# Optimization experiments

Measured on AMD Instinct MI355X. Metric: run time of the kernel, lower is better.

The kernel has to match this reference:

```python
import jax, jax.numpy as jnp
import numpy as np

TEMPERATURE = 0.1
EPS = 1e-8
NEG_INF = -9e15  # matches torch masked_fill value before temperature scaling


def setup_inputs() -> dict:
    key = jax.random.key(0)
    k1, k2 = jax.random.split(key)
    z1 = jax.random.normal(k1, (4096, 512), dtype=jnp.float32)
    z2 = jax.random.normal(k2, (4096, 512), dtype=jnp.float32)
    return {"z1": z1, "z2": z2}


def reference(z1, z2):
    feats = jnp.concatenate([z1, z2], axis=0)          # [2N, D]
    n2 = feats.shape[0]
    norms = jnp.linalg.norm(feats, axis=-1, keepdims=True)
    unit = feats / jnp.maximum(norms, EPS)             # cosine-normalized
    cos_sim = unit @ unit.T                            # [2N, 2N]
    idx = jnp.arange(n2)
    # mask self-similarity on the diagonal
    cos_sim = jnp.where(idx[:, None] == idx[None, :], NEG_INF, cos_sim)
    cos_sim = cos_sim / TEMPERATURE
    # positive for row i sits at column (i + N) mod 2N
    pos = cos_sim[idx, (idx + n2 // 2) % n2]           # [2N]
    nll = -pos + jax.scipy.special.logsumexp(cos_sim, axis=-1)
    return jnp.mean(nll)
```

## Files before the change

kernel.cpp:

```cpp
#include <hip/hip_runtime.h>
#include <hip/hip_bf16.h>
#include <math.h>

#define N2     8192
#define HALF_N 4096
#define DD     512
#define BM     128
#define BN     128
#define BKB    128
#define NKT    (DD / BKB)
#define NB     (N2 / BM)
#define NTRI   (NB * (NB + 1) / 2)

#define U_BYTES    ((size_t)N2 * DD)
#define PART_BYTES ((size_t)NB * N2 * 4)
#define PD_BYTES   ((size_t)HALF_N * 4)

typedef __attribute__((ext_vector_type(4))) float f32x4;
typedef __attribute__((ext_vector_type(4))) int   i32x4;
typedef __attribute__((ext_vector_type(8))) int   i32x8;

#define SCALE1 0x7F7F7F7F

__device__ __forceinline__ void load16_lds(const void* g, void* l) {
    __builtin_amdgcn_global_load_lds(
        (const __attribute__((address_space(1))) void*)g,
        (__attribute__((address_space(3))) void*)l, 16, 0, 0);
}

__global__ __launch_bounds__(256) void prep_kernel(
    const float* __restrict__ z1, const float* __restrict__ z2,
    unsigned char* __restrict__ U, float* __restrict__ out)
{
    const int tid = threadIdx.x;
    if (blockIdx.x == 0 && tid == 0) out[0] = 0.0f;

    const int wave = tid >> 6;
    const int lane = tid & 63;
    const int row  = blockIdx.x * 4 + wave;

    const float* src = (row < HALF_N) ? (z1 + (size_t)row * DD)
                                      : (z2 + (size_t)(row - HALF_N) * DD);
    float4 a = ((const float4*)src)[lane * 2 + 0];
    float4 b = ((const float4*)src)[lane * 2 + 1];
    float ss = a.x*a.x + a.y*a.y + a.z*a.z + a.w*a.w
             + b.x*b.x + b.y*b.y + b.z*b.z + b.w*b.w;
#pragma unroll
    for (int off = 32; off > 0; off >>= 1) ss += __shfl_xor(ss, off);
    const float inv = 1.0f / fmaxf(sqrtf(ss), 1e-8f);

    int lo = __builtin_amdgcn_cvt_pk_fp8_f32(a.x * inv, a.y * inv, 0,  0);
    lo     = __builtin_amdgcn_cvt_pk_fp8_f32(a.z * inv, a.w * inv, lo, 1);
    int hi = __builtin_amdgcn_cvt_pk_fp8_f32(b.x * inv, b.y * inv, 0,  0);
    hi     = __builtin_amdgcn_cvt_pk_fp8_f32(b.z * inv, b.w * inv, hi, 1);

    *(int2*)(U + (size_t)row * DD + lane * 8) = make_int2(lo, hi);
}

__global__ __launch_bounds__(256, 2) void gram_kernel(
    const unsigned char* __restrict__ U, float* __restrict__ partials,
    float* __restrict__ posdot)
{
    __shared__ unsigned char Ash[2][BM][BKB];
    __shared__ unsigned char Bsh[2][BN][BKB];
    __shared__ float racc[2][BM];
    __shared__ float cacc[2][BN];

    const int tid  = threadIdx.x;
    const int wave = tid >> 6;
    const int lane = tid & 63;

    const int t = blockIdx.x;
    int by = (int)((129.0 - sqrt(16641.0 - 8.0 * (double)t)) * 0.5);
    by = min(max(by, 0), NB - 1);
    while (by > 0       && t <  (by * (129 - by)) / 2) --by;
    while (by < NB - 1  && t >= ((by + 1) * (128 - by)) / 2) ++by;
    const int bx = by + (t - (by * (129 - by)) / 2);

    const int wr = wave >> 1;
    const int wc = wave & 1;
    const size_t arow0 = (size_t)by * BM;
    const size_t brow0 = (size_t)bx * BN;

    auto stage = [&](int kt, int buf) {
        const int k0 = kt * BKB;
        const int lr = lane >> 3;
        const int s  = (lane & 7) ^ (lr & 7);
#pragma unroll
        for (int hh = 0; hh < 4; ++hh) {
            const int c = wave * 4 + hh;
            const int r = c * 8 + lr;
            load16_lds(U + (arow0 + r) * DD + k0 + s * 16, &Ash[buf][c * 8][0]);
            load16_lds(U + (brow0 + r) * DD + k0 + s * 16, &Bsh[buf][c * 8][0]);
        }
    };

    f32x4 acc[4][4];
#pragma unroll
    for (int i = 0; i < 4; ++i)
#pragma unroll
        for (int j = 0; j < 4; ++j) acc[i][j] = (f32x4){0.f, 0.f, 0.f, 0.f};

    const int fr   = lane & 15;
    const int quad = lane >> 4;
    const int fr7  = fr & 7;
    const int t0   = (2 * quad) ^ fr7;
    const int t1   = t0 ^ 1;

    stage(0, 0);
    __syncthreads();

    for (int kt = 0; kt < NKT; ++kt) {
        const int buf = kt & 1;
        if (kt + 1 < NKT) stage(kt + 1, buf ^ 1);

        i32x8 af[4], bfr[4];
#pragma unroll
        for (int tt = 0; tt < 4; ++tt) {
            const int ar = wr * 64 + tt * 16 + fr;
            const int br = wc * 64 + tt * 16 + fr;
            i32x4 alo = *(const i32x4*)&Ash[buf][ar][t0 * 16];
            i32x4 ahi = *(const i32x4*)&Ash[buf][ar][t1 * 16];
            i32x4 blo = *(const i32x4*)&Bsh[buf][br][t0 * 16];
            i32x4 bhi = *(const i32x4*)&Bsh[buf][br][t1 * 16];
            af[tt]  = __builtin_shufflevector(alo, ahi, 0, 1, 2, 3, 4, 5, 6, 7);
            bfr[tt] = __builtin_shufflevector(blo, bhi, 0, 1, 2, 3, 4, 5, 6, 7);
        }
#pragma unroll
        for (int ct = 0; ct < 4; ++ct)
#pragma unroll
            for (int rt = 0; rt < 4; ++rt)
                acc[rt][ct] = __builtin_amdgcn_mfma_scale_f32_16x16x128_f8f6f4(
                                  af[rt], bfr[ct], acc[rt][ct],
                                  0, 0,
                                  0, SCALE1,
                                  0, SCALE1);
        __syncthreads();
    }

    const float SC = 14.42695040888963f;
    if (by == bx) {
#pragma unroll
        for (int rt = 0; rt < 4; ++rt) {
            const int lrow = wr * 64 + rt * 16 + quad * 4;
#pragma unroll
            for (int reg = 0; reg < 4; ++reg) {
                const int lr = lrow + reg;
                float s = 0.f;
#pragma unroll
                for (int ct = 0; ct < 4; ++ct) {
                    const int lc = wc * 64 + ct * 16 + fr;
                    const float e = exp2f(acc[rt][ct][reg] * SC);
                    s += (lc == lr) ? 0.f : e;
                }
                s += __shfl_xor(s, 1);
                s += __shfl_xor(s, 2);
                s += __shfl_xor(s, 4);
                s += __shfl_xor(s, 8);
                if (fr == 0) racc[wc][lr] = s;
            }
        }
    } else {
        float csum[4] = {0.f, 0.f, 0.f, 0.f};
#pragma unroll
        for (int rt = 0; rt < 4; ++rt) {
            const int lrow = wr * 64 + rt * 16 + quad * 4;
#pragma unroll
            for (int reg = 0; reg < 4; ++reg) {
                float s = 0.f;
#pragma unroll
                for (int ct = 0; ct < 4; ++ct) {
                    const float e = exp2f(acc[rt][ct][reg] * SC);
                    s += e;
                    csum[ct] += e;
                }
                s += __shfl_xor(s, 1);
                s += __shfl_xor(s, 2);
                s += __shfl_xor(s, 4);
                s += __shfl_xor(s, 8);
                if (fr == 0) racc[wc][lrow + reg] = s;
            }
        }
#pragma unroll
        for (int ct = 0; ct < 4; ++ct) {
            float c = csum[ct];
            c += __shfl_xor(c, 16);
            c += __shfl_xor(c, 32);
            if (quad == 0) cacc[wr][wc * 64 + ct * 16 + fr] = c;
        }
        if (posdot != nullptr && bx == by + 32 && wr == wc) {
#pragma unroll
            for (int rt = 0; rt < 4; ++rt) {
                const int lrow = rt * 16 + quad * 4;
#pragma unroll
                for (int reg = 0; reg < 4; ++reg)
                    if (fr == quad * 4 + reg)
                        posdot[arow0 + wr * 64 + lrow + reg] = acc[rt][rt][reg];
            }
        }
    }
    __syncthreads();

    if (tid < BM) {
        partials[(size_t)bx * N2 + arow0 + tid] = racc[0][tid] + racc[1][tid];
        if (by != bx)
            partials[(size_t)by * N2 + brow0 + tid] = cacc[0][tid] + cacc[1][tid];
    }
}

__global__ __launch_bounds__(256) void finalize_fast(
    const float* __restrict__ partials, const float* __restrict__ posdot,
    float* __restrict__ out)
{
    const int tid = threadIdx.x;
    const int row = blockIdx.x * 256 + tid;
    float s = 0.f;
#pragma unroll 8
    for (int j = 0; j < NB; ++j) s += partials[(size_t)j * N2 + row];
    float nll = -10.0f * posdot[row & (HALF_N - 1)] + logf(s);
#pragma unroll
    for (int off = 32; off > 0; off >>= 1) nll += __shfl_xor(nll, off);
    __shared__ float red[4];
    if ((tid & 63) == 0) red[tid >> 6] = nll;
    __syncthreads();
    if (tid == 0)
        atomicAdd(out, (red[0] + red[1] + red[2] + red[3]) * (1.0f / N2));
}

__device__ __forceinline__ float dec_e4m3(unsigned int b) {
    const int e = (b >> 3) & 15, m = b & 7;
    float v = e ? ldexpf((float)(8 + m), e - 10) : ldexpf((float)m, -9);
    return (b & 0x80u) ? -v : v;
}

__global__ __launch_bounds__(256) void finalize_slow(
    const unsigned char* __restrict__ U, const float* __restrict__ partials,
    float* __restrict__ out)
{
    const int tid  = threadIdx.x;
    const int wave = tid >> 6;
    const int lane = tid & 63;
    const int row  = blockIdx.x * 4 + wave;
    const int prow = (row + HALF_N) & (N2 - 1);

    uint2 xa = *(const uint2*)(U + (size_t)row  * DD + lane * 8);
    uint2 ya = *(const uint2*)(U + (size_t)prow * DD + lane * 8);
    float dot = 0.f;
#pragma unroll
    for (int j = 0; j < 4; ++j)
        dot += dec_e4m3(xa.x >> (8 * j)) * dec_e4m3(ya.x >> (8 * j));
#pragma unroll
    for (int j = 0; j < 4; ++j)
        dot += dec_e4m3(xa.y >> (8 * j)) * dec_e4m3(ya.y >> (8 * j));

    float ps = partials[(size_t)lane * N2 + row];
#pragma unroll
    for (int off = 32; off > 0; off >>= 1) {
        dot += __shfl_xor(dot, off);
        ps  += __shfl_xor(ps,  off);
    }
    __shared__ float part[4];
    if (lane == 0) part[wave] = -10.0f * dot + logf(ps);
    __syncthreads();
    if (tid == 0)
        atomicAdd(out, (part[0] + part[1] + part[2] + part[3]) * (1.0f / N2));
}

extern "C" void kernel_launch(void* const* d_in, const int* in_sizes, int n_in,
                              void* d_out, int out_size, void* d_ws, size_t ws_size,
                              hipStream_t stream)
{
    const float* z1 = (const float*)d_in[0];
    const float* z2 = (const float*)d_in[1];
    float* out      = (float*)d_out;
    unsigned char* U = (unsigned char*)d_ws;
    float* partials  = (float*)((char*)d_ws + U_BYTES);
    float* posdot    = (float*)((char*)d_ws + U_BYTES + PART_BYTES);
    const bool has_pd = ws_size >= U_BYTES + PART_BYTES + PD_BYTES;

    prep_kernel<<<N2 / 4, 256, 0, stream>>>(z1, z2, U, out);
    gram_kernel<<<NTRI, 256, 0, stream>>>(U, partials, has_pd ? posdot : nullptr);
    if (has_pd)
        finalize_fast<<<N2 / 256, 256, 0, stream>>>(partials, posdot, out);
    else
        finalize_slow<<<N2 / 4, 256, 0, stream>>>(U, partials, out);
}
```

Measured before the change: 114.2 us.

## Enlarge Gram tiles to 256x256 with 512-thread blocks and 64x128 wave tiles

Doubles the Gram-matrix block tile from 128x128 to 256x256 and launches 8 waves per block, each computing a 64x128 sub-tile that reuses its A fragments across 8 column tiles. The aim is to cut global-to-LDS and LDS-to-register traffic per MFMA and to shrink the number of triangular tile blocks and partial-sum rows. The triangular index math, diagonal masking, positive-pair extraction and column reductions are adapted to the new geometry. In exchange, LDS use rises to about 128KB per block, so likely only one block fits per CU. The 528 blocks also divide poorly across CUs, which may leave a load-imbalanced tail.

Measured after the change: 220.8 us. 93.3% more time.

```diff
diff --git a/kernel.cpp b/kernel.cpp
--- a/kernel.cpp
+++ b/kernel.cpp
@@ -5,8 +5,7 @@
 #define N2     8192
 #define HALF_N 4096
 #define DD     512
-#define BM     128
-#define BN     128
+#define BM     256
 #define BKB    128
 #define NKT    (DD / BKB)
 #define NB     (N2 / BM)
@@ -57,30 +56,30 @@
     *(int2*)(U + (size_t)row * DD + lane * 8) = make_int2(lo, hi);
 }
 
-__global__ __launch_bounds__(256, 2) void gram_kernel(
+__global__ __launch_bounds__(512, 2) void gram_kernel(
     const unsigned char* __restrict__ U, float* __restrict__ partials,
     float* __restrict__ posdot)
 {
     __shared__ unsigned char Ash[2][BM][BKB];
-    __shared__ unsigned char Bsh[2][BN][BKB];
+    __shared__ unsigned char Bsh[2][BM][BKB];
     __shared__ float racc[2][BM];
-    __shared__ float cacc[2][BN];
+    __shared__ float cacc[4][BM];
 
     const int tid  = threadIdx.x;
     const int wave = tid >> 6;
     const int lane = tid & 63;
 
     const int t = blockIdx.x;
-    int by = (int)((129.0 - sqrt(16641.0 - 8.0 * (double)t)) * 0.5);
+    int by = (int)((65.0 - sqrt(4225.0 - 8.0 * (double)t)) * 0.5);
     by = min(max(by, 0), NB - 1);
-    while (by > 0       && t <  (by * (129 - by)) / 2) --by;
-    while (by < NB - 1  && t >= ((by + 1) * (128 - by)) / 2) ++by;
-    const int bx = by + (t - (by * (129 - by)) / 2);
-
-    const int wr = wave >> 1;
-    const int wc = wave & 1;
+    while (by > 0       && t <  (by * (65 - by)) / 2) --by;
+    while (by < NB - 1  && t >= ((by + 1) * (64 - by)) / 2) ++by;
+    const int bx = by + (t - (by * (65 - by)) / 2);
+
+    const int wr2 = wave >> 1;
+    const int wcq = wave & 1;
     const size_t arow0 = (size_t)by * BM;
-    const size_t brow0 = (size_t)bx * BN;
+    const size_t brow0 = (size_t)bx * BM;
 
     auto stage = [&](int kt, int buf) {
         const int k0 = kt * BKB;
@@ -95,16 +94,15 @@
         }
     };
 
-    f32x4 acc[4][4];
+    f32x4 acc[4][8];
 #pragma unroll
     for (int i = 0; i < 4; ++i)
 #pragma unroll
-        for (int j = 0; j < 4; ++j) acc[i][j] = (f32x4){0.f, 0.f, 0.f, 0.f};
+        for (int j = 0; j < 8; ++j) acc[i][j] = (f32x4){0.f, 0.f, 0.f, 0.f};
 
     const int fr   = lane & 15;
     const int quad = lane >> 4;
-    const int fr7  = fr & 7;
-    const int t0   = (2 * quad) ^ fr7;
+    const int t0   = (2 * quad) ^ (fr & 7);
     const int t1   = t0 ^ 1;
 
     stage(0, 0);
@@ -114,27 +112,28 @@
         const int buf = kt & 1;
         if (kt + 1 < NKT) stage(kt + 1, buf ^ 1);
 
-        i32x8 af[4], bfr[4];
+        i32x8 af[4];
 #pragma unroll
         for (int tt = 0; tt < 4; ++tt) {
-            const int ar = wr * 64 + tt * 16 + fr;
-            const int br = wc * 64 + tt * 16 + fr;
+            const int ar = wr2 * 64 + tt * 16 + fr;
             i32x4 alo = *(const i32x4*)&Ash[buf][ar][t0 * 16];
             i32x4 ahi = *(const i32x4*)&Ash[buf][ar][t1 * 16];
+            af[tt] = __builtin_shufflevector(alo, ahi, 0, 1, 2, 3, 4, 5, 6, 7);
+        }
+#pragma unroll
+        for (int ct = 0; ct < 8; ++ct) {
+            const int br = wcq * 128 + ct * 16 + fr;
             i32x4 blo = *(const i32x4*)&Bsh[buf][br][t0 * 16];
             i32x4 bhi = *(const i32x4*)&Bsh[buf][br][t1 * 16];
-            af[tt]  = __builtin_shufflevector(alo, ahi, 0, 1, 2, 3, 4, 5, 6, 7);
-            bfr[tt] = __builtin_shufflevector(blo, bhi, 0, 1, 2, 3, 4, 5, 6, 7);
-        }
-#pragma unroll
-        for (int ct = 0; ct < 4; ++ct)
+            i32x8 bf  = __builtin_shufflevector(blo, bhi, 0, 1, 2, 3, 4, 5, 6, 7);
 #pragma unroll
             for (int rt = 0; rt < 4; ++rt)
                 acc[rt][ct] = __builtin_amdgcn_mfma_scale_f32_16x16x128_f8f6f4(
-                                  af[rt], bfr[ct], acc[rt][ct],
+                                  af[rt], bf, acc[rt][ct],
                                   0, 0,
                                   0, SCALE1,
                                   0, SCALE1);
+        }
         __syncthreads();
     }
 
@@ -142,14 +141,14 @@
     if (by == bx) {
 #pragma unroll
         for (int rt = 0; rt < 4; ++rt) {
-            const int lrow = wr * 64 + rt * 16 + quad * 4;
+            const int lrow = wr2 * 64 + rt * 16 + quad * 4;
 #pragma unroll
             for (int reg = 0; reg < 4; ++reg) {
                 const int lr = lrow + reg;
                 float s = 0.f;
 #pragma unroll
-                for (int ct = 0; ct < 4; ++ct) {
-                    const int lc = wc * 64 + ct * 16 + fr;
+                for (int ct = 0; ct < 8; ++ct) {
+                    const int lc = wcq * 128 + ct * 16 + fr;
                     const float e = exp2f(acc[rt][ct][reg] * SC);
                     s += (lc == lr) ? 0.f : e;
                 }
@@ -157,19 +156,19 @@
                 s += __shfl_xor(s, 2);
                 s += __shfl_xor(s, 4);
                 s += __shfl_xor(s, 8);
-                if (fr == 0) racc[wc][lr] = s;
+                if (fr == 0) racc[wcq][lr] = s;
             }
         }
     } else {
-        float csum[4] = {0.f, 0.f, 0.f, 0.f};
+        float csum[8] = {0.f, 0.f, 0.f, 0.f, 0.f, 0.f, 0.f, 0.f};
 #pragma unroll
         for (int rt = 0; rt < 4; ++rt) {
-            const int lrow = wr * 64 + rt * 16 + quad * 4;
+            const int lrow = wr2 * 64 + rt * 16 + quad * 4;
 #pragma unroll
             for (int reg = 0; reg < 4; ++reg) {
                 float s = 0.f;
 #pragma unroll
-                for (int ct = 0; ct < 4; ++ct) {
+                for (int ct = 0; ct < 8; ++ct) {
                     const float e = exp2f(acc[rt][ct][reg] * SC);
                     s += e;
                     csum[ct] += e;
@@ -178,24 +177,25 @@
                 s += __shfl_xor(s, 2);
                 s += __shfl_xor(s, 4);
                 s += __shfl_xor(s, 8);
-                if (fr == 0) racc[wc][lrow + reg] = s;
+                if (fr == 0) racc[wcq][lrow + reg] = s;
             }
         }
 #pragma unroll
-        for (int ct = 0; ct < 4; ++ct) {
+        for (int ct = 0; ct < 8; ++ct) {
             float c = csum[ct];
             c += __shfl_xor(c, 16);
             c += __shfl_xor(c, 32);
-            if (quad == 0) cacc[wr][wc * 64 + ct * 16 + fr] = c;
-        }
-        if (posdot != nullptr && bx == by + 32 && wr == wc) {
+            if (quad == 0) cacc[wr2][wcq * 128 + ct * 16 + fr] = c;
+        }
+        if (posdot != nullptr && bx == by + 16 && wcq == (wr2 >> 1)) {
 #pragma unroll
             for (int rt = 0; rt < 4; ++rt) {
-                const int lrow = rt * 16 + quad * 4;
+                const int lrow = wr2 * 64 + rt * 16 + quad * 4;
+                const int ct   = (wr2 & 1) * 4 + rt;
 #pragma unroll
                 for (int reg = 0; reg < 4; ++reg)
                     if (fr == quad * 4 + reg)
-                        posdot[arow0 + wr * 64 + lrow + reg] = acc[rt][rt][reg];
+                        posdot[arow0 + lrow + reg] = acc[rt][ct][reg];
             }
         }
     }
@@ -204,7 +204,8 @@
     if (tid < BM) {
         partials[(size_t)bx * N2 + arow0 + tid] = racc[0][tid] + racc[1][tid];
         if (by != bx)
-            partials[(size_t)by * N2 + brow0 + tid] = cacc[0][tid] + cacc[1][tid];
+            partials[(size_t)by * N2 + brow0 + tid] =
+                cacc[0][tid] + cacc[1][tid] + cacc[2][tid] + cacc[3][tid];
     }
 }
 
@@ -253,7 +254,7 @@
     for (int j = 0; j < 4; ++j)
         dot += dec_e4m3(xa.y >> (8 * j)) * dec_e4m3(ya.y >> (8 * j));
 
-    float ps = partials[(size_t)lane * N2 + row];
+    float ps = (lane < NB) ? partials[(size_t)lane * N2 + row] : 0.f;
 #pragma unroll
     for (int off = 32; off > 0; off >>= 1) {
         dot += __shfl_xor(dot, off);
@@ -279,7 +280,7 @@
     const bool has_pd = ws_size >= U_BYTES + PART_BYTES + PD_BYTES;
 
     prep_kernel<<<N2 / 4, 256, 0, stream>>>(z1, z2, U, out);
-    gram_kernel<<<NTRI, 256, 0, stream>>>(U, partials, has_pd ? posdot : nullptr);
+    gram_kernel<<<NTRI, 512, 0, stream>>>(U, partials, has_pd ? posdot : nullptr);
     if (has_pd)
         finalize_fast<<<N2 / 256, 256, 0, stream>>>(partials, posdot, out);
     else
```
